# Kernel tuning notes

Hardware: AMD Instinct MI355X
Metric: run time of the kernel (lower is better)

Reference implementation:

```python
import jax, jax.numpy as jnp
import numpy as np

B, S, D = 4, 2048, 1024
NEG = -1e10

def setup_inputs() -> dict:
    key = jax.random.key(0)
    ks = jax.random.split(key, 8)
    scale = 1.0 / np.sqrt(D)
    return {
        "hidden_states": jax.random.normal(ks[0], (B, S, D), jnp.float32),
        "mask": jax.random.randint(ks[1], (B, S), 0, 2, jnp.int32),
        "Wq": jax.random.normal(ks[2], (D, D), jnp.float32) * scale,
        "bq": jnp.zeros((D,), jnp.float32),
        "Wk": jax.random.normal(ks[3], (D, D), jnp.float32) * scale,
        "bk": jnp.zeros((D,), jnp.float32),
        "Wv": jax.random.normal(ks[4], (D, D), jnp.float32) * scale,
        "bv": jnp.zeros((D,), jnp.float32),
        "Wo": jax.random.normal(ks[5], (D, D), jnp.float32) * scale,
        "bo": jnp.zeros((D,), jnp.float32),
    }

def reference(hidden_states, mask, Wq, bq, Wk, bk, Wv, bv, Wo, bo):
    # torch Linear: y = x @ W.T + b
    q = jnp.einsum('bsd,ed->bse', hidden_states, Wq) + bq
    k = jnp.einsum('bsd,ed->bse', hidden_states, Wk) + bk
    v = jnp.einsum('bsd,ed->bse', hidden_states, Wv) + bv
    inv_sqrt_d = jnp.asarray(int(hidden_states.shape[-1]) ** (-0.5), hidden_states.dtype)
    weight = jnp.einsum('bqd,bkd->bqk', q, k) * inv_sqrt_d  # [B,S,S]
    # mask viewed as [B,1,S]: key-padding mask broadcast over query dim
    m = mask.reshape(mask.shape[0], 1, mask.shape[1])
    weight = jnp.where(m == 0, jnp.asarray(NEG, weight.dtype), weight)
    a = jax.nn.softmax(weight, axis=-1)
    hid = jnp.einsum('bqk,bkd->bqd', a, v)
    hid_o = jnp.einsum('bsd,ed->bse', hid, Wo) + bo
    return hidden_states + hid_o  # residual=True
```

## Files before the change

### kernel.cpp

```cpp
#include <hip/hip_runtime.h>
#include <stdint.h>


typedef __attribute__((ext_vector_type(8))) short bf16x8;
typedef __attribute__((ext_vector_type(4))) float f32x4;

typedef __attribute__((address_space(3))) void lds_void_t;
typedef __attribute__((address_space(1))) const void glb_void_t;

__device__ __forceinline__ ushort f2bf(float f) {
  uint32_t u = __float_as_uint(f);
  u += 0x7FFF + ((u >> 16) & 1);
  return (ushort)(u >> 16);
}
__device__ __forceinline__ float bf2f(ushort u) {
  return __uint_as_float(((uint32_t)u) << 16);
}

#define BAR   __builtin_amdgcn_s_barrier()
#define SCHED __builtin_amdgcn_sched_barrier(0)
#define LGKM0 asm volatile("s_waitcnt lgkmcnt(0)" ::: "memory")
#define VMC0  asm volatile("s_waitcnt vmcnt(0)" ::: "memory")
#define VMC4  asm volatile("s_waitcnt vmcnt(4)" ::: "memory")

__global__ __launch_bounds__(256) void convert_all(
    const float* __restrict__ X, const float* __restrict__ Wq,
    const float* __restrict__ Wk, const float* __restrict__ Wv,
    const float* __restrict__ Wo, const float* __restrict__ bq,
    const float* __restrict__ bk, const float* __restrict__ bv,
    ushort* __restrict__ Xb, ushort* __restrict__ Wqkvb,
    ushort* __restrict__ Wob, float* __restrict__ bqkv) {
  if (blockIdx.x >= 12288) {
#pragma unroll
    for (int u = 0; u < 3; ++u) {
      int base = (u * 256 + threadIdx.x) * 4;
      float4 v = (base < 1024)   ? *(const float4*)(bq + base)
               : (base < 2048)   ? *(const float4*)(bk + base - 1024)
                                 : *(const float4*)(bv + base - 2048);
      *(float4*)(bqkv + base) = v;
    }
    return;
  }
  int64_t o4 = ((int64_t)blockIdx.x * blockDim.x + threadIdx.x) * 4;
  const float* s; ushort* d; int64_t doff, soff;
  if (o4 < 8388608)        { s = X;  d = Xb;    doff = o4;            soff = o4; }
  else if (o4 < 9437184)   { s = Wq; d = Wqkvb; doff = o4 - 8388608;  soff = o4 - 8388608; }
  else if (o4 < 10485760)  { s = Wk; d = Wqkvb; doff = o4 - 8388608;  soff = o4 - 9437184; }
  else if (o4 < 11534336)  { s = Wv; d = Wqkvb; doff = o4 - 8388608;  soff = o4 - 10485760; }
  else                     { s = Wo; d = Wob;   doff = o4 - 11534336; soff = o4 - 11534336; }
  float4 v = *(const float4*)(s + soff);
  ushort4 o;
  o.x = f2bf(v.x); o.y = f2bf(v.y); o.z = f2bf(v.z); o.w = f2bf(v.w);
  *(ushort4*)(d + doff) = o;
}

#define BM 128
#define BKT 64

template <int MODE, int BNV, int GM>
__global__ __launch_bounds__(256) void gemm_bt(
    const ushort* __restrict__ Ag, const ushort* __restrict__ Bg,
    void* __restrict__ Og, const float* __restrict__ bias,
    const float* __restrict__ resid, ushort* __restrict__ Vt,
    const int* __restrict__ maskg, float* __restrict__ rowsum,
    int M, int N, int K, int lda, int ldb, int ldo,
    long long sAz, long long sBz, long long sOz, float scale) {
  constexpr int NFR = BNV / 32;
  __shared__ ushort LDSu[BM * BKT + BNV * BKT];
  ushort* const As = LDSu;
  ushort* const Bs = LDSu + BM * BKT;
  __shared__ int redn[4];

  const int z = blockIdx.z;
  const ushort* A = Ag + (int64_t)z * sAz;
  const ushort* B = Bg + (int64_t)z * sBz;

  const int tilesN = N / BNV;
  const int q8 = gridDim.x >> 3;
  const int wg = (blockIdx.x & 7) * q8 + (blockIdx.x >> 3);
  const int grpSz = GM * tilesN;
  const int tm = (wg / grpSz) * GM + (wg % GM);
  const int tn = (wg % grpSz) / GM;
  const int tid = threadIdx.x;
  const int wid = tid >> 6;
  const int lane = tid & 63;
  const int lr = lane & 15;
  const int kq = lane >> 4;
  const int wr = (wid >> 1) * 64;
  const int wc = (wid & 1) * (BNV / 2);

  if constexpr (MODE == 6) {
    const int4* mrow = (const int4*)(maskg + z * 2048);
    int4 ma = mrow[tid * 2];
    int4 mb = mrow[tid * 2 + 1];
    int cnt = (ma.x == 0) + (ma.y == 0) + (ma.z == 0) + (ma.w == 0) +
              (mb.x == 0) + (mb.y == 0) + (mb.z == 0) + (mb.w == 0);
#pragma unroll
    for (int off = 1; off < 64; off <<= 1) cnt += __shfl_xor(cnt, off);
    if (lane == 0) redn[wid] = cnt;
  }

  f32x4 acc[4][NFR];
#pragma unroll
  for (int m = 0; m < 4; ++m)
#pragma unroll
    for (int n = 0; n < NFR; ++n) acc[m][n] = (f32x4){0.f, 0.f, 0.f, 0.f};

  const int64_t abase = (int64_t)tm * BM;
  const int64_t bbase = (int64_t)tn * BNV;

  for (int kt = 0; kt < K; kt += BKT) {
    if (kt) __syncthreads();
#pragma unroll
    for (int r = 0; r < 4; ++r) {
      int idx = r * 256 + tid;
      int row = idx >> 3, slot = idx & 7;
      int sslot = slot ^ (row & 7);
      const ushort* ga = A + (abase + row) * lda + kt + sslot * 8;
      ushort* la = &As[(r * 256 + wid * 64) * 8];
      __builtin_amdgcn_global_load_lds((glb_void_t*)ga, (lds_void_t*)la, 16, 0, 0);
    }
#pragma unroll
    for (int r = 0; r < BNV / 32; ++r) {
      int idx = r * 256 + tid;
      int row = idx >> 3, slot = idx & 7;
      int sslot = slot ^ (row & 7);
      const ushort* gb = B + (bbase + row) * ldb + kt + sslot * 8;
      ushort* lb = &Bs[(r * 256 + wid * 64) * 8];
      __builtin_amdgcn_global_load_lds((glb_void_t*)gb, (lds_void_t*)lb, 16, 0, 0);
    }
    __syncthreads();

#pragma unroll
    for (int kk = 0; kk < 2; ++kk) {
      bf16x8 af[4], bfr[NFR];
#pragma unroll
      for (int m = 0; m < 4; ++m) {
        int row = wr + m * 16 + lr;
        int slot = (kk * 4 + kq) ^ (row & 7);
        af[m] = *(const bf16x8*)&As[row * 64 + slot * 8];
      }
#pragma unroll
      for (int n = 0; n < NFR; ++n) {
        int col = wc + n * 16 + lr;
        int slot = (kk * 4 + kq) ^ (col & 7);
        bfr[n] = *(const bf16x8*)&Bs[col * 64 + slot * 8];
      }
#pragma unroll
      for (int m = 0; m < 4; ++m)
#pragma unroll
        for (int n = 0; n < NFR; ++n)
          acc[m][n] = __builtin_amdgcn_mfma_f32_16x16x32_bf16(af[m], bfr[n], acc[m][n], 0, 0, 0);
    }
  }

  if constexpr (MODE == 6) {
    float nm = (float)(redn[0] + redn[1] + redn[2] + redn[3]);
    float invr[4][4];
#pragma unroll
    for (int m = 0; m < 4; ++m)
#pragma unroll
      for (int i = 0; i < 4; ++i)
        invr[m][i] =
            1.0f / (rowsum[z * 2048 + tm * BM + wr + m * 16 + kq * 4 + i] - nm);
#pragma unroll
    for (int m = 0; m < 4; ++m) {
      int r0 = tm * BM + wr + m * 16 + kq * 4;
#pragma unroll
      for (int n = 0; n < NFR; ++n) {
        int c = tn * BNV + wc + n * 16 + lr;
#pragma unroll
        for (int i = 0; i < 4; ++i)
          ((ushort*)Og)[(int64_t)z * sOz + (int64_t)(r0 + i) * ldo + c] =
              f2bf(acc[m][n][i] * invr[m][i]);
      }
    }
  } else if constexpr (MODE == 4) {
    if (tn < 8) {
#pragma unroll
      for (int m = 0; m < 4; ++m) {
        int r0 = tm * BM + wr + m * 16 + kq * 4;
#pragma unroll
        for (int n = 0; n < NFR; ++n) {
          int c = tn * BNV + wc + n * 16 + lr;
          const float bb = bias[c];
#pragma unroll
          for (int i = 0; i < 4; ++i)
            ((ushort*)Og)[(int64_t)(r0 + i) * 2048 + c] =
                f2bf((acc[m][n][i] + bb) * 0.03125f);
        }
      }
    } else if (tn < 16) {
#pragma unroll
      for (int m = 0; m < 4; ++m) {
        int r0 = tm * BM + wr + m * 16 + kq * 4;
        int4 mv = *(const int4*)(maskg + r0);
        int mk[4] = {mv.x, mv.y, mv.z, mv.w};
#pragma unroll
        for (int n = 0; n < NFR; ++n) {
          int c = tn * BNV + wc + n * 16 + lr;
          const float bb = bias[c];
#pragma unroll
          for (int i = 0; i < 4; ++i)
            ((ushort*)Og)[(int64_t)(r0 + i) * 2048 + c] =
                mk[i] ? f2bf(acc[m][n][i] + bb) : (ushort)0;
        }
      }
    } else {
      __syncthreads();
#pragma unroll
      for (int m = 0; m < 4; ++m) {
        int rl0 = wr + m * 16 + kq * 4;
        int4 mv = *(const int4*)(maskg + tm * BM + rl0);
        int mk[4] = {mv.x, mv.y, mv.z, mv.w};
#pragma unroll
        for (int n = 0; n < NFR; ++n) {
          int cl = wc + n * 16 + lr;
          const float bb = bias[tn * BNV + cl];
#pragma unroll
          for (int i = 0; i < 4; ++i) {
            int rl = rl0 + i;
            ushort v = mk[i] ? f2bf(acc[m][n][i] + bb) : (ushort)0;
            LDSu[cl * 128 + (rl ^ ((cl & 7) << 3))] = v;
          }
        }
      }
      __syncthreads();
      {
        const int e = tid >> 1, h = tid & 1;
        ushort* dst = Vt + (int64_t)((tn - 16) * BNV + e) * 8192 + tm * BM + h * 64;
        const ushort* src = &LDSu[e * 128 + h * 64];
#pragma unroll
        for (int g = 0; g < 8; ++g) {
          bf16x8 vv = *(const bf16x8*)&src[((g ^ (e & 7)) & 7) * 8];
          *(bf16x8*)&dst[g * 8] = vv;
        }
      }
    }
  } else {
#pragma unroll
    for (int m = 0; m < 4; ++m) {
      int r0 = tm * BM + wr + m * 16 + kq * 4;
#pragma unroll
      for (int n = 0; n < NFR; ++n) {
        int c = tn * BNV + wc + n * 16 + lr;
        const float bb = bias[c];
#pragma unroll
        for (int i = 0; i < 4; ++i) {
          int rrow = r0 + i;
          ((float*)Og)[(int64_t)rrow * ldo + c] =
              acc[m][n][i] + bb + resid[(int64_t)rrow * ldo + c];
        }
      }
    }
  }
}

__global__ __launch_bounds__(512, 2) void scores8(
    const ushort* __restrict__ QKg, ushort* __restrict__ P,
    float* __restrict__ rowsum) {
  __shared__ ushort AsU[32768];
  __shared__ ushort BsU[32768];

  const int z = blockIdx.z;
  const ushort* Ab = QKg + (int64_t)z * (2048 * 2048);
  const ushort* Bb = Ab + 1024;
  const int64_t zoff = (int64_t)z * (2048 * 2048);

  const int q8 = gridDim.x >> 3;
  const int wg = (blockIdx.x & 7) * q8 + (blockIdx.x >> 3);
  const int tm = wg >> 3, tn = wg & 7;

  const int tid = threadIdx.x;
  const int wid = tid >> 6, lane = tid & 63;
  const int lr = lane & 15, kq = lane >> 4;
  const int wrh = wid >> 2;
  const int wcq = wid & 3;
  const int hB = wcq >> 1;
  const int wcin = (wcq & 1) * 64;

  const int r0 = tid >> 3;
  const int g0 = ((tid & 7) ^ (r0 & 7)) * 8;
  const ushort* gA = Ab + (int64_t)(tm * 256 + r0) * 2048 + g0;
  const ushort* gB = Bb + (int64_t)(tn * 256 + r0) * 2048 + g0;

#define SGA(BUF, H, KT) do {                                                   \
    __builtin_amdgcn_global_load_lds(                                          \
        (glb_void_t*)(gA + (int64_t)((H) * 128) * 2048 + (KT)),                \
        (lds_void_t*)(AsU + (((BUF) * 2 + (H)) * 1024 + tid) * 8), 16, 0, 0);  \
    __builtin_amdgcn_global_load_lds(                                          \
        (glb_void_t*)(gA + (int64_t)((H) * 128 + 64) * 2048 + (KT)),           \
        (lds_void_t*)(AsU + (((BUF) * 2 + (H)) * 1024 + 512 + tid) * 8), 16, 0, 0); \
  } while (0)
#define SGB(BUF, H, KT) do {                                                   \
    __builtin_amdgcn_global_load_lds(                                          \
        (glb_void_t*)(gB + (int64_t)((H) * 128) * 2048 + (KT)),                \
        (lds_void_t*)(BsU + (((BUF) * 2 + (H)) * 1024 + tid) * 8), 16, 0, 0);  \
    __builtin_amdgcn_global_load_lds(                                          \
        (glb_void_t*)(gB + (int64_t)((H) * 128 + 64) * 2048 + (KT)),           \
        (lds_void_t*)(BsU + (((BUF) * 2 + (H)) * 1024 + 512 + tid) * 8), 16, 0, 0); \
  } while (0)

  const int rsw0 = (kq ^ (lr & 7)) * 8;
  const int rsw1 = rsw0 ^ 32;

  bf16x8 a[4][2], bb[4][2];
  f32x4 acc[8][4];
#pragma unroll
  for (int m = 0; m < 8; ++m)
#pragma unroll
    for (int n = 0; n < 4; ++n) acc[m][n] = (f32x4){0.f, 0.f, 0.f, 0.f};

#define RDA1(BUF, MH, MQ) {                                                    \
    int rr = ((MH) * 4 + (MQ)) * 16 + lr;                                      \
    const ushort* p_ = AsU + ((BUF) * 2 + wrh) * 8192 + rr * 64;               \
    a[MQ][0] = *(const bf16x8*)(p_ + rsw0);                                    \
    a[MQ][1] = *(const bf16x8*)(p_ + rsw1); }
#define RDA(BUF, MH) RDA1(BUF, MH, 0) RDA1(BUF, MH, 1) RDA1(BUF, MH, 2) RDA1(BUF, MH, 3)
#define RDB1(BUF, NH, NQ) {                                                    \
    int n_ = (NH) * 2 + (NQ);                                                  \
    int cc = wcin + n_ * 16 + lr;                                              \
    const ushort* p_ = BsU + ((BUF) * 2 + hB) * 8192 + cc * 64;                \
    bb[n_][0] = *(const bf16x8*)(p_ + rsw0);                                   \
    bb[n_][1] = *(const bf16x8*)(p_ + rsw1); }
#define RDB(BUF, NH) RDB1(BUF, NH, 0) RDB1(BUF, NH, 1)
#define MM2X(MH, MQ, N) \
    acc[(MH)*4+(MQ)][N] = __builtin_amdgcn_mfma_f32_16x16x32_bf16(a[MQ][0], bb[N][0], acc[(MH)*4+(MQ)][N], 0, 0, 0); \
    acc[(MH)*4+(MQ)][N] = __builtin_amdgcn_mfma_f32_16x16x32_bf16(a[MQ][1], bb[N][1], acc[(MH)*4+(MQ)][N], 0, 0, 0);
#define CL8(MH, NH) \
    __builtin_amdgcn_s_setprio(1); \
    MM2X(MH, 0, (NH)*2) MM2X(MH, 0, (NH)*2+1) MM2X(MH, 1, (NH)*2) MM2X(MH, 1, (NH)*2+1) \
    MM2X(MH, 2, (NH)*2) MM2X(MH, 2, (NH)*2+1) MM2X(MH, 3, (NH)*2) MM2X(MH, 3, (NH)*2+1) \
    __builtin_amdgcn_s_setprio(0);

  SGA(0, 0, 0); SGA(0, 1, 0); SGB(0, 0, 0); SGB(0, 1, 0);
  SGB(1, 0, 64); SGB(1, 1, 64);
  VMC4; BAR; SCHED;

  for (int it = 0; it < 8; ++it) {
    const bool last = (it == 7);
    const int ktA1 = it * 128 + 64;
    const int ktN = it * 128 + 128;
    const int ktN1 = it * 128 + 192;
    RDA(0, 0) RDB(0, 0)
    SGA(1, 0, ktA1);
    BAR; LGKM0; SCHED;
    CL8(0, 0)
    SCHED; BAR;
    RDB(0, 1)
    SGA(1, 1, ktA1);
    BAR; LGKM0; SCHED;
    CL8(0, 1)
    SCHED; BAR;
    RDA(0, 1)
    if (!last) { SGB(0, 0, ktN); }
    BAR; LGKM0; SCHED;
    CL8(1, 1)
    SCHED; BAR;
    if (!last) { SGB(0, 1, ktN); }
    CL8(1, 0)
    SCHED;
    if (last) { VMC0; } else { VMC4; }
    BAR;
    RDA(1, 0) RDB(1, 0)
    if (!last) { SGA(0, 0, ktN); }
    BAR; LGKM0; SCHED;
    CL8(0, 0)
    SCHED; BAR;
    RDB(1, 1)
    if (!last) { SGA(0, 1, ktN); }
    BAR; LGKM0; SCHED;
    CL8(0, 1)
    SCHED; BAR;
    RDA(1, 1)
    if (!last) { SGB(1, 0, ktN1); }
    BAR; LGKM0; SCHED;
    CL8(1, 1)
    SCHED; BAR;
    if (!last) { SGB(1, 1, ktN1); }
    CL8(1, 0)
    SCHED;
    if (!last) { VMC4; BAR; }
  }

  float part[8][4];
#pragma unroll
  for (int m = 0; m < 8; ++m)
#pragma unroll
    for (int i = 0; i < 4; ++i) part[m][i] = 0.f;
  const int colb = tn * 256 + wcq * 64;
#pragma unroll
  for (int m = 0; m < 8; ++m) {
    const int rl = wrh * 128 + m * 16 + kq * 4;
#pragma unroll
    for (int n = 0; n < 4; ++n) {
      const int c = colb + n * 16 + lr;
#pragma unroll
      for (int i = 0; i < 4; ++i) {
        float e = __expf(acc[m][n][i]);
        P[zoff + (int64_t)(tm * 256 + rl + i) * 2048 + c] = f2bf(e);
        part[m][i] += e;
      }
    }
  }
#pragma unroll
  for (int off = 1; off <= 8; off <<= 1)
#pragma unroll
    for (int m = 0; m < 8; ++m)
#pragma unroll
      for (int i = 0; i < 4; ++i)
        part[m][i] += __shfl_xor(part[m][i], off);
  float* pbuf = (float*)AsU;
  if (lr == 0) {
#pragma unroll
    for (int m = 0; m < 8; ++m)
#pragma unroll
      for (int i = 0; i < 4; ++i)
        pbuf[wcq * 256 + wrh * 128 + m * 16 + kq * 4 + i] = part[m][i];
  }
  __syncthreads();
  if (tid < 256) {
    float s = pbuf[tid] + pbuf[256 + tid] + pbuf[512 + tid] + pbuf[768 + tid];
    atomicAdd(&rowsum[z * 2048 + tm * 256 + tid], s);
  }
#undef SGA
#undef SGB
#undef RDA1
#undef RDA
#undef RDB1
#undef RDB
#undef MM2X
#undef CL8
}

extern "C" void kernel_launch(void* const* d_in, const int* in_sizes, int n_in,
                              void* d_out, int out_size, void* d_ws, size_t ws_size,
                              hipStream_t stream) {
  const float* hs = (const float*)d_in[0];
  const int* mask = (const int*)d_in[1];
  const float* Wq = (const float*)d_in[2];
  const float* bq = (const float*)d_in[3];
  const float* Wk = (const float*)d_in[4];
  const float* bk = (const float*)d_in[5];
  const float* Wv = (const float*)d_in[6];
  const float* bv = (const float*)d_in[7];
  const float* Wo = (const float*)d_in[8];
  const float* bo = (const float*)d_in[9];
  float* out = (float*)d_out;
  char* w = (char*)d_ws;

  ushort* Xb    = (ushort*)(w + 0);
  float*  rowsum = (float*)(w + 0);
  ushort* Wqkvb = (ushort*)(w + 16777216);
  ushort* Wob   = (ushort*)(w + 23068672);
  ushort* QKb   = (ushort*)(w + 25165824);
  ushort* Vt    = (ushort*)(w + 58720256);
  ushort* P     = (ushort*)(w + 75497472);
  float*  bqkv  = (float*)(w + 92274688);
  ushort* AO    = (ushort*)(w + 109051904);

  convert_all<<<12289, 256, 0, stream>>>(hs, Wq, Wk, Wv, Wo, bq, bk, bv,
                                         Xb, Wqkvb, Wob, bqkv);

  gemm_bt<4, 128, 8><<<dim3(1536, 1, 1), 256, 0, stream>>>(Xb, Wqkvb, QKb, bqkv,
      nullptr, Vt, mask, nullptr,
      8192, 3072, 1024, 1024, 1024, 2048, 0, 0, 0, 1.f);

  hipMemsetAsync(rowsum, 0, 8192 * sizeof(float), stream);

  scores8<<<dim3(64, 1, 4), 512, 0, stream>>>(QKb, P, rowsum);

  gemm_bt<6, 128, 4><<<dim3(128, 1, 4), 256, 0, stream>>>(P, Vt, AO, nullptr,
      nullptr, nullptr, mask, rowsum,
      2048, 1024, 2048, 2048, 8192, 1024,
      (long long)2048 * 2048, (long long)2048, (long long)2048 * 1024, 1.f);

  gemm_bt<3, 64, 8><<<dim3(1024, 1, 1), 256, 0, stream>>>(AO, Wob, (void*)out, bo,
      hs, nullptr, nullptr, nullptr,
      8192, 1024, 1024, 1024, 1024, 1024, 0, 0, 0, 1.f);
}
```

Before: 177.8 us.

## Replace QKV projection GEMM with 256x256-tile 8-wave pipelined kernel sharing scores loop

Moves the K-loop into a shared macro and adds a qkv8 kernel that computes the fused QKV projection with 256x256 tiles, 512 threads and the same double-buffered global-to-LDS pipeline used by the scores kernel. It replaces the generic 128-wide gemm_bt MODE 4 launch. The epilogue keeps the earlier behaviour: Q is scaled, K is masked, and V is masked and transposed through LDS. The larger tiles raise data reuse and cut the number of blocks. The trade-off is a grid of 384 blocks, which may fill the CUs unevenly, and the V-transpose epilogue now has to fit a 256x256 tile in LDS.

```diff
diff --git a/kernel.cpp b/kernel.cpp
--- a/kernel.cpp
+++ b/kernel.cpp
@@ -175,68 +175,6 @@
               f2bf(acc[m][n][i] * invr[m][i]);
       }
     }
-  } else if constexpr (MODE == 4) {
-    if (tn < 8) {
-#pragma unroll
-      for (int m = 0; m < 4; ++m) {
-        int r0 = tm * BM + wr + m * 16 + kq * 4;
-#pragma unroll
-        for (int n = 0; n < NFR; ++n) {
-          int c = tn * BNV + wc + n * 16 + lr;
-          const float bb = bias[c];
-#pragma unroll
-          for (int i = 0; i < 4; ++i)
-            ((ushort*)Og)[(int64_t)(r0 + i) * 2048 + c] =
-                f2bf((acc[m][n][i] + bb) * 0.03125f);
-        }
-      }
-    } else if (tn < 16) {
-#pragma unroll
-      for (int m = 0; m < 4; ++m) {
-        int r0 = tm * BM + wr + m * 16 + kq * 4;
-        int4 mv = *(const int4*)(maskg + r0);
-        int mk[4] = {mv.x, mv.y, mv.z, mv.w};
-#pragma unroll
-        for (int n = 0; n < NFR; ++n) {
-          int c = tn * BNV + wc + n * 16 + lr;
-          const float bb = bias[c];
-#pragma unroll
-          for (int i = 0; i < 4; ++i)
-            ((ushort*)Og)[(int64_t)(r0 + i) * 2048 + c] =
-                mk[i] ? f2bf(acc[m][n][i] + bb) : (ushort)0;
-        }
-      }
-    } else {
-      __syncthreads();
-#pragma unroll
-      for (int m = 0; m < 4; ++m) {
-        int rl0 = wr + m * 16 + kq * 4;
-        int4 mv = *(const int4*)(maskg + tm * BM + rl0);
-        int mk[4] = {mv.x, mv.y, mv.z, mv.w};
-#pragma unroll
-        for (int n = 0; n < NFR; ++n) {
-          int cl = wc + n * 16 + lr;
-          const float bb = bias[tn * BNV + cl];
-#pragma unroll
-          for (int i = 0; i < 4; ++i) {
-            int rl = rl0 + i;
-            ushort v = mk[i] ? f2bf(acc[m][n][i] + bb) : (ushort)0;
-            LDSu[cl * 128 + (rl ^ ((cl & 7) << 3))] = v;
-          }
-        }
-      }
-      __syncthreads();
-      {
-        const int e = tid >> 1, h = tid & 1;
-        ushort* dst = Vt + (int64_t)((tn - 16) * BNV + e) * 8192 + tm * BM + h * 64;
-        const ushort* src = &LDSu[e * 128 + h * 64];
-#pragma unroll
-        for (int g = 0; g < 8; ++g) {
-          bf16x8 vv = *(const bf16x8*)&src[((g ^ (e & 7)) & 7) * 8];
-          *(bf16x8*)&dst[g * 8] = vv;
-        }
-      }
-    }
   } else {
 #pragma unroll
     for (int m = 0; m < 4; ++m) {
@@ -256,61 +194,22 @@
   }
 }
 
-__global__ __launch_bounds__(512, 2) void scores8(
-    const ushort* __restrict__ QKg, ushort* __restrict__ P,
-    float* __restrict__ rowsum) {
-  __shared__ ushort AsU[32768];
-  __shared__ ushort BsU[32768];
-
-  const int z = blockIdx.z;
-  const ushort* Ab = QKg + (int64_t)z * (2048 * 2048);
-  const ushort* Bb = Ab + 1024;
-  const int64_t zoff = (int64_t)z * (2048 * 2048);
-
-  const int q8 = gridDim.x >> 3;
-  const int wg = (blockIdx.x & 7) * q8 + (blockIdx.x >> 3);
-  const int tm = wg >> 3, tn = wg & 7;
-
-  const int tid = threadIdx.x;
-  const int wid = tid >> 6, lane = tid & 63;
-  const int lr = lane & 15, kq = lane >> 4;
-  const int wrh = wid >> 2;
-  const int wcq = wid & 3;
-  const int hB = wcq >> 1;
-  const int wcin = (wcq & 1) * 64;
-
-  const int r0 = tid >> 3;
-  const int g0 = ((tid & 7) ^ (r0 & 7)) * 8;
-  const ushort* gA = Ab + (int64_t)(tm * 256 + r0) * 2048 + g0;
-  const ushort* gB = Bb + (int64_t)(tn * 256 + r0) * 2048 + g0;
-
 #define SGA(BUF, H, KT) do {                                                   \
     __builtin_amdgcn_global_load_lds(                                          \
-        (glb_void_t*)(gA + (int64_t)((H) * 128) * 2048 + (KT)),                \
+        (glb_void_t*)(gA + (int64_t)((H) * 128) * LDAB + (KT)),                \
         (lds_void_t*)(AsU + (((BUF) * 2 + (H)) * 1024 + tid) * 8), 16, 0, 0);  \
     __builtin_amdgcn_global_load_lds(                                          \
-        (glb_void_t*)(gA + (int64_t)((H) * 128 + 64) * 2048 + (KT)),           \
+        (glb_void_t*)(gA + (int64_t)((H) * 128 + 64) * LDAB + (KT)),           \
         (lds_void_t*)(AsU + (((BUF) * 2 + (H)) * 1024 + 512 + tid) * 8), 16, 0, 0); \
   } while (0)
 #define SGB(BUF, H, KT) do {                                                   \
     __builtin_amdgcn_global_load_lds(                                          \
-        (glb_void_t*)(gB + (int64_t)((H) * 128) * 2048 + (KT)),                \
+        (glb_void_t*)(gB + (int64_t)((H) * 128) * LDAB + (KT)),                \
         (lds_void_t*)(BsU + (((BUF) * 2 + (H)) * 1024 + tid) * 8), 16, 0, 0);  \
     __builtin_amdgcn_global_load_lds(                                          \
-        (glb_void_t*)(gB + (int64_t)((H) * 128 + 64) * 2048 + (KT)),           \
+        (glb_void_t*)(gB + (int64_t)((H) * 128 + 64) * LDAB + (KT)),           \
         (lds_void_t*)(BsU + (((BUF) * 2 + (H)) * 1024 + 512 + tid) * 8), 16, 0, 0); \
   } while (0)
-
-  const int rsw0 = (kq ^ (lr & 7)) * 8;
-  const int rsw1 = rsw0 ^ 32;
-
-  bf16x8 a[4][2], bb[4][2];
-  f32x4 acc[8][4];
-#pragma unroll
-  for (int m = 0; m < 8; ++m)
-#pragma unroll
-    for (int n = 0; n < 4; ++n) acc[m][n] = (f32x4){0.f, 0.f, 0.f, 0.f};
-
 #define RDA1(BUF, MH, MQ) {                                                    \
     int rr = ((MH) * 4 + (MQ)) * 16 + lr;                                      \
     const ushort* p_ = AsU + ((BUF) * 2 + wrh) * 8192 + rr * 64;               \
@@ -333,55 +232,96 @@
     MM2X(MH, 2, (NH)*2) MM2X(MH, 2, (NH)*2+1) MM2X(MH, 3, (NH)*2) MM2X(MH, 3, (NH)*2+1) \
     __builtin_amdgcn_s_setprio(0);
 
-  SGA(0, 0, 0); SGA(0, 1, 0); SGB(0, 0, 0); SGB(0, 1, 0);
-  SGB(1, 0, 64); SGB(1, 1, 64);
-  VMC4; BAR; SCHED;
-
-  for (int it = 0; it < 8; ++it) {
-    const bool last = (it == 7);
-    const int ktA1 = it * 128 + 64;
-    const int ktN = it * 128 + 128;
-    const int ktN1 = it * 128 + 192;
-    RDA(0, 0) RDB(0, 0)
-    SGA(1, 0, ktA1);
-    BAR; LGKM0; SCHED;
-    CL8(0, 0)
-    SCHED; BAR;
-    RDB(0, 1)
-    SGA(1, 1, ktA1);
-    BAR; LGKM0; SCHED;
-    CL8(0, 1)
-    SCHED; BAR;
-    RDA(0, 1)
-    if (!last) { SGB(0, 0, ktN); }
-    BAR; LGKM0; SCHED;
-    CL8(1, 1)
-    SCHED; BAR;
-    if (!last) { SGB(0, 1, ktN); }
-    CL8(1, 0)
-    SCHED;
-    if (last) { VMC0; } else { VMC4; }
-    BAR;
-    RDA(1, 0) RDB(1, 0)
-    if (!last) { SGA(0, 0, ktN); }
-    BAR; LGKM0; SCHED;
-    CL8(0, 0)
-    SCHED; BAR;
-    RDB(1, 1)
-    if (!last) { SGA(0, 1, ktN); }
-    BAR; LGKM0; SCHED;
-    CL8(0, 1)
-    SCHED; BAR;
-    RDA(1, 1)
-    if (!last) { SGB(1, 0, ktN1); }
-    BAR; LGKM0; SCHED;
-    CL8(1, 1)
-    SCHED; BAR;
-    if (!last) { SGB(1, 1, ktN1); }
-    CL8(1, 0)
-    SCHED;
-    if (!last) { VMC4; BAR; }
-  }
+#define KLOOP8                                                                  \
+  SGA(0, 0, 0); SGA(0, 1, 0); SGB(0, 0, 0); SGB(0, 1, 0);                       \
+  SGB(1, 0, 64); SGB(1, 1, 64);                                                 \
+  VMC4; BAR; SCHED;                                                             \
+  for (int it = 0; it < 8; ++it) {                                              \
+    const bool last = (it == 7);                                                \
+    const int ktA1 = it * 128 + 64;                                             \
+    const int ktN = it * 128 + 128;                                             \
+    const int ktN1 = it * 128 + 192;                                            \
+    RDA(0, 0) RDB(0, 0)                                                         \
+    SGA(1, 0, ktA1);                                                            \
+    BAR; LGKM0; SCHED;                                                          \
+    CL8(0, 0)                                                                   \
+    SCHED; BAR;                                                                 \
+    RDB(0, 1)                                                                   \
+    SGA(1, 1, ktA1);                                                            \
+    BAR; LGKM0; SCHED;                                                          \
+    CL8(0, 1)                                                                   \
+    SCHED; BAR;                                                                 \
+    RDA(0, 1)                                                                   \
+    if (!last) { SGB(0, 0, ktN); }                                              \
+    BAR; LGKM0; SCHED;                                                          \
+    CL8(1, 1)                                                                   \
+    SCHED; BAR;                                                                 \
+    if (!last) { SGB(0, 1, ktN); }                                              \
+    CL8(1, 0)                                                                   \
+    SCHED;                                                                      \
+    if (last) { VMC0; } else { VMC4; }                                          \
+    BAR;                                                                        \
+    RDA(1, 0) RDB(1, 0)                                                         \
+    if (!last) { SGA(0, 0, ktN); }                                              \
+    BAR; LGKM0; SCHED;                                                          \
+    CL8(0, 0)                                                                   \
+    SCHED; BAR;                                                                 \
+    RDB(1, 1)                                                                   \
+    if (!last) { SGA(0, 1, ktN); }                                              \
+    BAR; LGKM0; SCHED;                                                          \
+    CL8(0, 1)                                                                   \
+    SCHED; BAR;                                                                 \
+    RDA(1, 1)                                                                   \
+    if (!last) { SGB(1, 0, ktN1); }                                             \
+    BAR; LGKM0; SCHED;                                                          \
+    CL8(1, 1)                                                                   \
+    SCHED; BAR;                                                                 \
+    if (!last) { SGB(1, 1, ktN1); }                                             \
+    CL8(1, 0)                                                                   \
+    SCHED;                                                                      \
+    if (!last) { VMC4; BAR; }                                                   \
+  }
+
+__global__ __launch_bounds__(512, 2) void scores8(
+    const ushort* __restrict__ QKg, ushort* __restrict__ P,
+    float* __restrict__ rowsum) {
+  __shared__ ushort AsU[32768];
+  __shared__ ushort BsU[32768];
+  constexpr int LDAB = 2048;
+
+  const int z = blockIdx.z;
+  const ushort* Ab = QKg + (int64_t)z * (2048 * 2048);
+  const ushort* Bb = Ab + 1024;
+  const int64_t zoff = (int64_t)z * (2048 * 2048);
+
+  const int q8 = gridDim.x >> 3;
+  const int wg = (blockIdx.x & 7) * q8 + (blockIdx.x >> 3);
+  const int tm = wg >> 3, tn = wg & 7;
+
+  const int tid = threadIdx.x;
+  const int wid = tid >> 6, lane = tid & 63;
+  const int lr = lane & 15, kq = lane >> 4;
+  const int wrh = wid >> 2;
+  const int wcq = wid & 3;
+  const int hB = wcq >> 1;
+  const int wcin = (wcq & 1) * 64;
+
+  const int r0 = tid >> 3;
+  const int g0 = ((tid & 7) ^ (r0 & 7)) * 8;
+  const ushort* gA = Ab + (int64_t)(tm * 256 + r0) * LDAB + g0;
+  const ushort* gB = Bb + (int64_t)(tn * 256 + r0) * LDAB + g0;
+
+  const int rsw0 = (kq ^ (lr & 7)) * 8;
+  const int rsw1 = rsw0 ^ 32;
+
+  bf16x8 a[4][2], bb[4][2];
+  f32x4 acc[8][4];
+#pragma unroll
+  for (int m = 0; m < 8; ++m)
+#pragma unroll
+    for (int n = 0; n < 4; ++n) acc[m][n] = (f32x4){0.f, 0.f, 0.f, 0.f};
+
+  KLOOP8
 
   float part[8][4];
 #pragma unroll
@@ -423,6 +363,105 @@
     float s = pbuf[tid] + pbuf[256 + tid] + pbuf[512 + tid] + pbuf[768 + tid];
     atomicAdd(&rowsum[z * 2048 + tm * 256 + tid], s);
   }
+}
+
+__global__ __launch_bounds__(512, 2) void qkv8(
+    const ushort* __restrict__ Xg, const ushort* __restrict__ Wg,
+    ushort* __restrict__ QKb, const float* __restrict__ bias,
+    ushort* __restrict__ Vt, const int* __restrict__ maskg) {
+  __shared__ ushort LDS2[65536];
+  ushort* const AsU = LDS2;
+  ushort* const BsU = LDS2 + 32768;
+  constexpr int LDAB = 1024;
+
+  const int q8 = gridDim.x >> 3;
+  const int wg = (blockIdx.x & 7) * q8 + (blockIdx.x >> 3);
+  const int tm = (wg / 48) * 4 + (wg & 3);
+  const int tn = (wg % 48) >> 2;
+
+  const int tid = threadIdx.x;
+  const int wid = tid >> 6, lane = tid & 63;
+  const int lr = lane & 15, kq = lane >> 4;
+  const int wrh = wid >> 2;
+  const int wcq = wid & 3;
+  const int hB = wcq >> 1;
+  const int wcin = (wcq & 1) * 64;
+
+  const int r0 = tid >> 3;
+  const int g0 = ((tid & 7) ^ (r0 & 7)) * 8;
+  const ushort* gA = Xg + (int64_t)(tm * 256 + r0) * LDAB + g0;
+  const ushort* gB = Wg + (int64_t)(tn * 256 + r0) * LDAB + g0;
+
+  const int rsw0 = (kq ^ (lr & 7)) * 8;
+  const int rsw1 = rsw0 ^ 32;
+
+  bf16x8 a[4][2], bb[4][2];
+  f32x4 acc[8][4];
+#pragma unroll
+  for (int m = 0; m < 8; ++m)
+#pragma unroll
+    for (int n = 0; n < 4; ++n) acc[m][n] = (f32x4){0.f, 0.f, 0.f, 0.f};
+
+  KLOOP8
+
+  const int clw = wcq * 64;
+  if (tn < 8) {
+    const float qscale = (tn < 4) ? 0.03125f : 1.0f;
+    const bool isK = (tn >= 4);
+#pragma unroll
+    for (int m = 0; m < 8; ++m) {
+      const int rg = tm * 256 + wrh * 128 + m * 16 + kq * 4;
+      int mk[4] = {1, 1, 1, 1};
+      if (isK) {
+        int4 mv = *(const int4*)(maskg + rg);
+        mk[0] = mv.x; mk[1] = mv.y; mk[2] = mv.z; mk[3] = mv.w;
+      }
+#pragma unroll
+      for (int n = 0; n < 4; ++n) {
+        const int c = tn * 256 + clw + n * 16 + lr;
+        const float bbv = bias[c];
+#pragma unroll
+        for (int i = 0; i < 4; ++i) {
+          ushort v = mk[i] ? f2bf((acc[m][n][i] + bbv) * qscale) : (ushort)0;
+          QKb[(int64_t)(rg + i) * 2048 + c] = v;
+        }
+      }
+    }
+  } else {
+    BAR;
+#pragma unroll
+    for (int m = 0; m < 8; ++m) {
+      const int rl0 = wrh * 128 + m * 16 + kq * 4;
+      int4 mv = *(const int4*)(maskg + tm * 256 + rl0);
+      int mk[4] = {mv.x, mv.y, mv.z, mv.w};
+#pragma unroll
+      for (int n = 0; n < 4; ++n) {
+        const int cl = clw + n * 16 + lr;
+        const float bbv = bias[tn * 256 + cl];
+#pragma unroll
+        for (int i = 0; i < 4; ++i) {
+          const int rl = rl0 + i;
+          ushort v = mk[i] ? f2bf(acc[m][n][i] + bbv) : (ushort)0;
+          LDS2[cl * 256 + (rl ^ ((cl & 7) << 3))] = v;
+        }
+      }
+    }
+    BAR;
+    {
+      const int e = tid >> 1, h = tid & 1;
+      const int sw = (e & 7) << 3;
+      ushort* dst = Vt + (int64_t)((tn - 8) * 256 + e) * 8192 + tm * 256 + h * 128;
+      const ushort* src = &LDS2[e * 256];
+#pragma unroll
+      for (int g = 0; g < 16; ++g) {
+        const int tb8 = h * 128 + g * 8;
+        bf16x8 vv = *(const bf16x8*)&src[tb8 ^ sw];
+        *(bf16x8*)&dst[g * 8] = vv;
+      }
+    }
+  }
+}
+
 #undef SGA
 #undef SGB
 #undef RDA1
@@ -431,7 +470,7 @@
 #undef RDB
 #undef MM2X
 #undef CL8
-}
+#undef KLOOP8
 
 extern "C" void kernel_launch(void* const* d_in, const int* in_sizes, int n_in,
                               void* d_out, int out_size, void* d_ws, size_t ws_size,
@@ -462,9 +501,7 @@
   convert_all<<<12289, 256, 0, stream>>>(hs, Wq, Wk, Wv, Wo, bq, bk, bv,
                                          Xb, Wqkvb, Wob, bqkv);
 
-  gemm_bt<4, 128, 8><<<dim3(1536, 1, 1), 256, 0, stream>>>(Xb, Wqkvb, QKb, bqkv,
-      nullptr, Vt, mask, nullptr,
-      8192, 3072, 1024, 1024, 1024, 2048, 0, 0, 0, 1.f);
+  qkv8<<<dim3(384, 1, 1), 512, 0, stream>>>(Xb, Wqkvb, QKb, bqkv, Vt, mask);
 
   hipMemsetAsync(rowsum, 0, 8192 * sizeof(float), stream);
 
```

After: 199.4 us. 1.12x slower.
